# Optimization experiments

Hardware: AMD Instinct MI355X
Metric: run time of the kernel (lower is better)

Reference implementation:

```python
import jax, jax.numpy as jnp
import numpy as np

N_EMBED = 1024
N_HEAD = 16
B, T = 4, 2048
EPS = 1e-5


def setup_inputs() -> dict:
    key = jax.random.key(0)
    ks = jax.random.split(key, 8)
    s = 0.02
    return {
        "x": jax.random.normal(ks[0], (B, T, N_EMBED), dtype=jnp.float32),
        "ln1_w": jnp.ones((N_EMBED,), jnp.float32),
        "ln1_b": jnp.zeros((N_EMBED,), jnp.float32),
        "w_qkv": jax.random.normal(ks[1], (N_EMBED, 3 * N_EMBED), dtype=jnp.float32) * s,
        "b_qkv": jnp.zeros((3 * N_EMBED,), jnp.float32),
        "w_o": jax.random.normal(ks[2], (N_EMBED, N_EMBED), dtype=jnp.float32) * s,
        "b_o": jnp.zeros((N_EMBED,), jnp.float32),
        "ln2_w": jnp.ones((N_EMBED,), jnp.float32),
        "ln2_b": jnp.zeros((N_EMBED,), jnp.float32),
        "w_fc": jax.random.normal(ks[3], (N_EMBED, 4 * N_EMBED), dtype=jnp.float32) * s,
        "b_fc": jnp.zeros((4 * N_EMBED,), jnp.float32),
        "w_proj": jax.random.normal(ks[4], (4 * N_EMBED, N_EMBED), dtype=jnp.float32) * s,
        "b_proj": jnp.zeros((N_EMBED,), jnp.float32),
    }


def _layernorm(x, w, b):
    mu = jnp.mean(x, axis=-1, keepdims=True)
    var = jnp.mean(jnp.square(x - mu), axis=-1, keepdims=True)
    return (x - mu) * jax.lax.rsqrt(var + EPS) * w + b


def _attention(x, w_qkv, b_qkv, w_o, b_o):
    b, t, c = x.shape
    hd = c // N_HEAD
    qkv = x @ w_qkv + b_qkv                      # [B,T,3C]
    q, k, v = jnp.split(qkv, 3, axis=-1)
    # [B,H,T,hd]
    q = q.reshape(b, t, N_HEAD, hd).transpose(0, 2, 1, 3)
    k = k.reshape(b, t, N_HEAD, hd).transpose(0, 2, 1, 3)
    v = v.reshape(b, t, N_HEAD, hd).transpose(0, 2, 1, 3)
    scale = 1.0 / np.sqrt(hd).astype(np.float32)
    scores = jnp.einsum('bhqd,bhkd->bhqk', q, k) * scale  # [B,H,T,T]
    mask = jnp.tril(jnp.ones((t, t), dtype=bool))
    scores = jnp.where(mask, scores, -jnp.inf)
    attn = jax.nn.softmax(scores, axis=-1)
    ctx = jnp.einsum('bhqk,bhkd->bhqd', attn, v)  # [B,H,T,hd]
    ctx = ctx.transpose(0, 2, 1, 3).reshape(b, t, c)
    return ctx @ w_o + b_o


def reference(x, ln1_w, ln1_b, w_qkv, b_qkv, w_o, b_o,
              ln2_w, ln2_b, w_fc, b_fc, w_proj, b_proj):
    # x = x + attn(ln1(x))
    x = x + _attention(_layernorm(x, ln1_w, ln1_b), w_qkv, b_qkv, w_o, b_o)
    # x = x + mlp(ln2(x))
    h = _layernorm(x, ln2_w, ln2_b)
    h = jax.nn.gelu(h @ w_fc + b_fc, approximate=False)
    x = x + (h @ w_proj + b_proj)
    return x
```

## Files before the change

### kernel.cpp

```cpp
#include <hip/hip_runtime.h>
#include <hip/hip_bf16.h>
#include <math.h>

#define N_EMBED 1024
#define N_HEAD 16
#define HD 64
#define BB 4
#define TT 2048
#define NTOK (BB * TT)
#define QKV_LD (3 * N_EMBED)

typedef __bf16 bf16x8 __attribute__((ext_vector_type(8)));
typedef float f32x4 __attribute__((ext_vector_type(4)));

__device__ __forceinline__ unsigned short f2bf(float f) {
    __hip_bfloat16 h = __float2bfloat16(f);
    return __builtin_bit_cast(unsigned short, h);
}

__device__ __forceinline__ void gll16(const unsigned short* g, unsigned short* l) {
    __builtin_amdgcn_global_load_lds(
        (const __attribute__((address_space(1))) void*)g,
        (__attribute__((address_space(3))) void*)l,
        16, 0, 0);
}

__global__ __launch_bounds__(256) void transpose_bf16_kernel(
    const float* __restrict__ in, unsigned short* __restrict__ out, int K, int N) {
    __shared__ float tile[32][33];
    int bx = blockIdx.x * 32;
    int by = blockIdx.y * 32;
    int tx = threadIdx.x, ty = threadIdx.y;
#pragma unroll
    for (int i = ty; i < 32; i += 8)
        tile[i][tx] = in[(size_t)(by + i) * N + bx + tx];
    __syncthreads();
#pragma unroll
    for (int i = ty; i < 32; i += 8)
        out[(size_t)(bx + i) * K + by + tx] = f2bf(tile[tx][i]);
}

__global__ __launch_bounds__(256) void transpose_v_kernel(
    const unsigned short* __restrict__ qkv, unsigned short* __restrict__ vt) {
    __shared__ unsigned short tile[32][33];
    int z = blockIdx.z;
    int b = z >> 4, h = z & 15;
    int t0 = blockIdx.x * 32, d0 = blockIdx.y * 32;
    int tx = threadIdx.x, ty = threadIdx.y;
    const unsigned short* src = qkv + (size_t)(b * TT) * QKV_LD + 2 * N_EMBED + h * HD;
#pragma unroll
    for (int i = ty; i < 32; i += 8)
        tile[i][tx] = src[(size_t)(t0 + i) * QKV_LD + d0 + tx];
    __syncthreads();
    unsigned short* dst = vt + (size_t)z * HD * TT;
#pragma unroll
    for (int i = ty; i < 32; i += 8)
        dst[(size_t)(d0 + i) * TT + t0 + tx] = tile[tx][i];
}

__global__ __launch_bounds__(256) void ln_kernel(
    const float* __restrict__ x, const float* __restrict__ w,
    const float* __restrict__ b, unsigned short* __restrict__ out) {
    int row = blockIdx.x;
    int t = threadIdx.x;
    const float* xr = x + (size_t)row * N_EMBED;
    float4 v = reinterpret_cast<const float4*>(xr)[t];
    float s = v.x + v.y + v.z + v.w;
    float s2 = v.x * v.x + v.y * v.y + v.z * v.z + v.w * v.w;
#pragma unroll
    for (int m = 1; m < 64; m <<= 1) {
        s += __shfl_xor(s, m);
        s2 += __shfl_xor(s2, m);
    }
    __shared__ float red[8];
    int wv = t >> 6, ln = t & 63;
    if (ln == 0) { red[wv] = s; red[wv + 4] = s2; }
    __syncthreads();
    s = red[0] + red[1] + red[2] + red[3];
    s2 = red[4] + red[5] + red[6] + red[7];
    float mu = s * (1.0f / N_EMBED);
    float var = s2 * (1.0f / N_EMBED) - mu * mu;
    float r = rsqrtf(var + 1e-5f);
    float4 wv4 = reinterpret_cast<const float4*>(w)[t];
    float4 bv4 = reinterpret_cast<const float4*>(b)[t];
    ushort4 o;
    o.x = f2bf((v.x - mu) * r * wv4.x + bv4.x);
    o.y = f2bf((v.y - mu) * r * wv4.y + bv4.y);
    o.z = f2bf((v.z - mu) * r * wv4.z + bv4.z);
    o.w = f2bf((v.w - mu) * r * wv4.w + bv4.w);
    *reinterpret_cast<ushort4*>(out + (size_t)row * N_EMBED + t * 4) = o;
}

template <int EPI>
__global__ __launch_bounds__(256) void gemm_kernel(
    const unsigned short* __restrict__ A,
    const unsigned short* __restrict__ BT,
    const float* __restrict__ bias,
    const float* __restrict__ resid,
    float* __restrict__ outf,
    unsigned short* __restrict__ outb,
    int M, int N, int K) {
    __shared__ __align__(16) unsigned short As[3][128 * 32];
    __shared__ __align__(16) unsigned short Bs[3][128 * 32];
    int nbn = N >> 7;
    int nwg = gridDim.x;
    int orig = blockIdx.x;
    int swz = (orig & 7) * (nwg >> 3) + (orig >> 3);
    int bm = swz / nbn, bn = swz % nbn;
    int t = threadIdx.x;
    int lane = t & 63, wv = t >> 6;
    int wm = wv >> 1, wn = wv & 1;
    int mr = lane & 15, kg = lane >> 4;

    f32x4 acc[4][4];
#pragma unroll
    for (int i = 0; i < 4; i++)
#pragma unroll
        for (int j = 0; j < 4; j++) acc[i][j] = (f32x4){0.f, 0.f, 0.f, 0.f};

    int srow = t >> 2, sq = t & 3;
    int sqs = sq ^ ((srow >> 1) & 3);
    const unsigned short* gA1 = A + (size_t)(bm * 128 + srow) * K + sqs * 8;
    const unsigned short* gA2 = gA1 + (size_t)64 * K;
    const unsigned short* gB1 = BT + (size_t)(bn * 128 + srow) * K + sqs * 8;
    const unsigned short* gB2 = gB1 + (size_t)64 * K;
    int w512 = wv * 512;

    auto stageg = [&](int ki, int bi) {
        int k0 = ki << 5;
        gll16(gA1 + k0, As[bi] + w512);
        gll16(gA2 + k0, As[bi] + 2048 + w512);
        gll16(gB1 + k0, Bs[bi] + w512);
        gll16(gB2 + k0, Bs[bi] + 2048 + w512);
    };

    int nk = K >> 5;
    stageg(0, 0);
    stageg(1, 1);

    const int csw = (mr >> 1) & 3;
    for (int ki = 0; ki < nk; ki++) {
        if (ki + 1 < nk) {
            asm volatile("s_waitcnt vmcnt(4)" ::: "memory");
        } else {
            asm volatile("s_waitcnt vmcnt(0)" ::: "memory");
        }
        __builtin_amdgcn_s_barrier();
        if (ki + 2 < nk) stageg(ki + 2, (ki + 2) % 3);

        int cur = ki % 3;
        bf16x8 af[4], bfr[4];
#pragma unroll
        for (int i = 0; i < 4; i++)
            af[i] = *reinterpret_cast<const bf16x8*>(
                &As[cur][(wm * 64 + i * 16 + mr) * 32 + ((kg ^ csw) * 8)]);
#pragma unroll
        for (int j = 0; j < 4; j++)
            bfr[j] = *reinterpret_cast<const bf16x8*>(
                &Bs[cur][(wn * 64 + j * 16 + mr) * 32 + ((kg ^ csw) * 8)]);
#pragma unroll
        for (int i = 0; i < 4; i++)
#pragma unroll
            for (int j = 0; j < 4; j++)
                acc[i][j] = __builtin_amdgcn_mfma_f32_16x16x32_bf16(af[i], bfr[j], acc[i][j], 0, 0, 0);
    }

#pragma unroll
    for (int i = 0; i < 4; i++)
#pragma unroll
        for (int j = 0; j < 4; j++) {
            int n = bn * 128 + wn * 64 + j * 16 + mr;
            float bs = bias[n];
#pragma unroll
            for (int r = 0; r < 4; r++) {
                int m = bm * 128 + wm * 64 + i * 16 + kg * 4 + r;
                size_t idx = (size_t)m * N + n;
                float v = acc[i][j][r] + bs;
                if (EPI == 0) {
                    outb[idx] = f2bf(v);
                } else if (EPI == 1) {
                    outf[idx] = v + resid[idx];
                } else {
                    float g = 0.5f * v * (1.0f + erff(v * 0.70710678118f));
                    outb[idx] = f2bf(g);
                }
            }
        }
}

__global__ __launch_bounds__(256) void attn_kernel(
    const unsigned short* __restrict__ qkv,
    const unsigned short* __restrict__ vt,
    unsigned short* __restrict__ ctx) {
    __shared__ __align__(16) unsigned short Kb[3][4096];
    __shared__ __align__(16) unsigned short Vb[3][4096];
    __shared__ __align__(16) unsigned short PT[8192];
    const float SCL = 0.18033688011112042f;
    int t = threadIdx.x, lane = t & 63, wv = t >> 6;
    int mr = lane & 15, kg = lane >> 4;

    int wid = blockIdx.x;
    int bh = wid & 63, qp2 = wid >> 6;
    int h = bh & 15, b = bh >> 4;

    const unsigned short* qptr = qkv + (size_t)(b * TT) * QKV_LD + h * HD;
    const unsigned short* kp = qptr + N_EMBED;
    const unsigned short* vtp = vt + (size_t)bh * HD * TT;

    int srow[2], scol[2], sbase[2];
#pragma unroll
    for (int i = 0; i < 2; i++) {
        int L = i * 256 + wv * 64 + lane;
        int row = L >> 3, slot = L & 7;
        srow[i] = row;
        scol[i] = (slot ^ (row & 7)) * 8;
        sbase[i] = (i * 256 + wv * 64) * 8;
    }
    const int csw = mr & 7;

    auto stage = [&](int tile, int bi) {
        int kv0 = tile * 64;
#pragma unroll
        for (int i = 0; i < 2; i++) {
            gll16(kp + (size_t)(kv0 + srow[i]) * QKV_LD + scol[i], &Kb[bi][sbase[i]]);
            gll16(vtp + (size_t)srow[i] * TT + kv0 + scol[i], &Vb[bi][sbase[i]]);
        }
    };

    for (int item = 0; item < 2; ++item) {
        int qt = (item == 0) ? qp2 : 15 - qp2;
        int ntiles = 2 * qt + 2;
        int qbase = qt * 128 + wv * 32;

        bf16x8 aq[2][2];
#pragma unroll
        for (int f = 0; f < 2; f++)
#pragma unroll
            for (int c = 0; c < 2; c++)
                aq[f][c] = *reinterpret_cast<const bf16x8*>(
                    qptr + (size_t)(qbase + f * 16 + mr) * QKV_LD + c * 32 + kg * 8);

        f32x4 Oa[2][4];
#pragma unroll
        for (int f = 0; f < 2; f++)
#pragma unroll
            for (int jd = 0; jd < 4; jd++) Oa[f][jd] = (f32x4){0.f, 0.f, 0.f, 0.f};
        float mrow[2] = {-3.0e38f, -3.0e38f};
        float lrow[2] = {0.f, 0.f};

        stage(0, 0);
        stage(1, 1);

        for (int tl = 0; tl < ntiles; ++tl) {
            if (tl + 1 < ntiles) {
                asm volatile("s_waitcnt vmcnt(4)" ::: "memory");
            } else {
                asm volatile("s_waitcnt vmcnt(0)" ::: "memory");
            }
            __builtin_amdgcn_s_barrier();
            int t2 = tl + 2;
            if (t2 < ntiles) stage(t2, t2 % 3);

            int bi = tl % 3;
            int kv0 = tl * 64;
            const unsigned short* Kt = Kb[bi];
            const unsigned short* Vt = Vb[bi];

            f32x4 sf[2][4];
#pragma unroll
            for (int j = 0; j < 4; j++) {
                int rl = j * 16 + mr;
                bf16x8 bk0 = *reinterpret_cast<const bf16x8*>(&Kt[rl * 64 + (kg ^ csw) * 8]);
                bf16x8 bk1 = *reinterpret_cast<const bf16x8*>(&Kt[rl * 64 + ((4 + kg) ^ csw) * 8]);
#pragma unroll
                for (int f = 0; f < 2; f++) {
                    f32x4 s = (f32x4){0.f, 0.f, 0.f, 0.f};
                    s = __builtin_amdgcn_mfma_f32_16x16x32_bf16(bk0, aq[f][0], s, 0, 0, 0);
                    s = __builtin_amdgcn_mfma_f32_16x16x32_bf16(bk1, aq[f][1], s, 0, 0, 0);
                    sf[f][j] = s;
                }
            }

            bool dmask = (tl >= 2 * qt);
#pragma unroll
            for (int f = 0; f < 2; f++) {
                int qrow = qbase + f * 16 + mr;
                int R = wv * 32 + f * 16 + mr;
                float mx = -3.0e38f;
#pragma unroll
                for (int j = 0; j < 4; j++)
#pragma unroll
                    for (int r = 0; r < 4; r++) {
                        float sv = sf[f][j][r] * SCL;
                        if (dmask && (kv0 + j * 16 + kg * 4 + r > qrow)) sv = -3.0e38f;
                        sf[f][j][r] = sv;
                        mx = fmaxf(mx, sv);
                    }
                mx = fmaxf(mx, __shfl_xor(mx, 16));
                mx = fmaxf(mx, __shfl_xor(mx, 32));
                float mn = fmaxf(mrow[f], mx);
                float al = __builtin_amdgcn_exp2f(mrow[f] - mn);
                mrow[f] = mn;
#pragma unroll
                for (int jd = 0; jd < 4; jd++) Oa[f][jd] *= al;
                float ps = 0.f;
#pragma unroll
                for (int j = 0; j < 4; j++)
#pragma unroll
                    for (int r = 0; r < 4; r++) {
                        float p = __builtin_amdgcn_exp2f(sf[f][j][r] - mn);
                        sf[f][j][r] = p;
                        ps += p;
                    }
                ps += __shfl_xor(ps, 16);
                ps += __shfl_xor(ps, 32);
                lrow[f] = lrow[f] * al + ps;
                int rsw = R & 7;
#pragma unroll
                for (int j = 0; j < 4; j++) {
                    unsigned lo = (unsigned)f2bf(sf[f][j][0]) | ((unsigned)f2bf(sf[f][j][1]) << 16);
                    unsigned hi = (unsigned)f2bf(sf[f][j][2]) | ((unsigned)f2bf(sf[f][j][3]) << 16);
                    int cw = 2 * j + (kg >> 1);
                    int addr = R * 64 + ((cw ^ rsw) << 3) + (kg & 1) * 4;
                    uint2 pk; pk.x = lo; pk.y = hi;
                    *reinterpret_cast<uint2*>(&PT[addr]) = pk;
                }
            }

#pragma unroll
            for (int c = 0; c < 2; c++) {
                int R0 = wv * 32 + mr, R1 = R0 + 16;
                bf16x8 pb0 = *reinterpret_cast<const bf16x8*>(
                    &PT[R0 * 64 + (((c * 4 + kg) ^ (R0 & 7)) << 3)]);
                bf16x8 pb1 = *reinterpret_cast<const bf16x8*>(
                    &PT[R1 * 64 + (((c * 4 + kg) ^ (R1 & 7)) << 3)]);
#pragma unroll
                for (int jd = 0; jd < 4; jd++) {
                    int rv = jd * 16 + mr;
                    bf16x8 vf = *reinterpret_cast<const bf16x8*>(
                        &Vt[rv * 64 + (((c * 4 + kg) ^ (rv & 7)) << 3)]);
                    Oa[0][jd] = __builtin_amdgcn_mfma_f32_16x16x32_bf16(vf, pb0, Oa[0][jd], 0, 0, 0);
                    Oa[1][jd] = __builtin_amdgcn_mfma_f32_16x16x32_bf16(vf, pb1, Oa[1][jd], 0, 0, 0);
                }
            }
        }

#pragma unroll
        for (int f = 0; f < 2; f++) {
            float iv = 1.0f / lrow[f];
            int q = qbase + f * 16 + mr;
#pragma unroll
            for (int jd = 0; jd < 4; jd++) {
                ushort4 o;
                o.x = f2bf(Oa[f][jd][0] * iv);
                o.y = f2bf(Oa[f][jd][1] * iv);
                o.z = f2bf(Oa[f][jd][2] * iv);
                o.w = f2bf(Oa[f][jd][3] * iv);
                *reinterpret_cast<ushort4*>(
                    ctx + (size_t)(b * TT + q) * N_EMBED + h * HD + jd * 16 + kg * 4) = o;
            }
        }
        __syncthreads();
    }
}

extern "C" void kernel_launch(void* const* d_in, const int* in_sizes, int n_in,
                              void* d_out, int out_size, void* d_ws, size_t ws_size,
                              hipStream_t stream) {
    const float* x      = (const float*)d_in[0];
    const float* ln1_w  = (const float*)d_in[1];
    const float* ln1_b  = (const float*)d_in[2];
    const float* w_qkv  = (const float*)d_in[3];
    const float* b_qkv  = (const float*)d_in[4];
    const float* w_o    = (const float*)d_in[5];
    const float* b_o    = (const float*)d_in[6];
    const float* ln2_w  = (const float*)d_in[7];
    const float* ln2_b  = (const float*)d_in[8];
    const float* w_fc   = (const float*)d_in[9];
    const float* b_fc   = (const float*)d_in[10];
    const float* w_proj = (const float*)d_in[11];
    const float* b_proj = (const float*)d_in[12];
    float* out = (float*)d_out;

    char* ws = (char*)d_ws;
    size_t off = 0;
    auto alloc = [&](size_t bytes) -> void* {
        void* p = ws + off;
        off += (bytes + 255) & ~(size_t)255;
        return p;
    };
    unsigned short* wqkv_t  = (unsigned short*)alloc((size_t)3072 * 1024 * 2);
    unsigned short* wo_t    = (unsigned short*)alloc((size_t)1024 * 1024 * 2);
    unsigned short* wfc_t   = (unsigned short*)alloc((size_t)4096 * 1024 * 2);
    unsigned short* wproj_t = (unsigned short*)alloc((size_t)1024 * 4096 * 2);
    unsigned short* lnb     = (unsigned short*)alloc((size_t)NTOK * 1024 * 2);
    float*          x1      = (float*)alloc((size_t)NTOK * 1024 * 4);
    unsigned short* qkv     = (unsigned short*)alloc((size_t)NTOK * 3072 * 2);
    unsigned short* ctxb    = (unsigned short*)alloc((size_t)NTOK * 1024 * 2);
    unsigned short* hbuf    = qkv;
    unsigned short* vt      = (unsigned short*)x1;

    dim3 tb32(32, 8);
    transpose_bf16_kernel<<<dim3(3072 / 32, 1024 / 32), tb32, 0, stream>>>(w_qkv, wqkv_t, 1024, 3072);
    transpose_bf16_kernel<<<dim3(1024 / 32, 1024 / 32), tb32, 0, stream>>>(w_o, wo_t, 1024, 1024);
    transpose_bf16_kernel<<<dim3(4096 / 32, 1024 / 32), tb32, 0, stream>>>(w_fc, wfc_t, 1024, 4096);
    transpose_bf16_kernel<<<dim3(1024 / 32, 4096 / 32), tb32, 0, stream>>>(w_proj, wproj_t, 4096, 1024);

    ln_kernel<<<NTOK, 256, 0, stream>>>(x, ln1_w, ln1_b, lnb);
    gemm_kernel<0><<<(NTOK / 128) * (3072 / 128), 256, 0, stream>>>(
        lnb, wqkv_t, b_qkv, nullptr, nullptr, qkv, NTOK, 3072, 1024);
    transpose_v_kernel<<<dim3(TT / 32, HD / 32, BB * N_HEAD), tb32, 0, stream>>>(qkv, vt);
    attn_kernel<<<512, 256, 0, stream>>>(qkv, vt, ctxb);
    gemm_kernel<1><<<(NTOK / 128) * (1024 / 128), 256, 0, stream>>>(
        ctxb, wo_t, b_o, x, x1, nullptr, NTOK, 1024, 1024);
    ln_kernel<<<NTOK, 256, 0, stream>>>(x1, ln2_w, ln2_b, lnb);
    gemm_kernel<2><<<(NTOK / 128) * (4096 / 128), 256, 0, stream>>>(
        lnb, wfc_t, b_fc, nullptr, nullptr, hbuf, NTOK, 4096, 1024);
    gemm_kernel<1><<<(NTOK / 128) * (1024 / 128), 256, 0, stream>>>(
        hbuf, wproj_t, b_proj, x1, out, nullptr, NTOK, 1024, 4096);
}
```

Measured before the change: 425.1 us.

## Enlarge GEMM tiles to 256x256/256x128 with templated warp layout and MFMA priority

Replaces the fixed 128x128 GEMM with a templated kernel where each wave computes a 128x64 output tile (8x4 MFMA accumulators). The QKV and FC GEMMs use 256x256 tiles with 512 threads, and the O and proj GEMMs use 256x128 tiles. The aim is more operand reuse per LDS load and less global traffic per FLOP. It also raises wave priority around the MFMA block with s_setprio. The cost is higher register pressure, since accumulators double, plus more LDS per block and fewer blocks for the N=1024 GEMMs, which may hurt occupancy and tail balance.

```diff
diff --git a/kernel.cpp b/kernel.cpp
--- a/kernel.cpp
+++ b/kernel.cpp
@@ -91,8 +91,8 @@
     *reinterpret_cast<ushort4*>(out + (size_t)row * N_EMBED + t * 4) = o;
 }
 
-template <int EPI>
-__global__ __launch_bounds__(256) void gemm_kernel(
+template <int EPI, int WM, int WN>
+__global__ __launch_bounds__(WM * WN * 64, 2) void gemm256_kernel(
     const unsigned short* __restrict__ A,
     const unsigned short* __restrict__ BT,
     const float* __restrict__ bias,
@@ -100,80 +100,103 @@
     float* __restrict__ outf,
     unsigned short* __restrict__ outb,
     int M, int N, int K) {
-    __shared__ __align__(16) unsigned short As[3][128 * 32];
-    __shared__ __align__(16) unsigned short Bs[3][128 * 32];
-    int nbn = N >> 7;
+    constexpr int BM = WM * 128;
+    constexpr int BN = WN * 64;
+    constexpr int T = WM * WN * 64;
+    constexpr int CA = BM * 4 / T;
+    constexpr int CB = BN * 4 / T;
+    constexpr int CALLS = CA + CB;
+    __shared__ __align__(16) unsigned short As[3][BM * 32];
+    __shared__ __align__(16) unsigned short Bs[3][BN * 32];
+
+    int nbn = N / BN;
     int nwg = gridDim.x;
     int orig = blockIdx.x;
     int swz = (orig & 7) * (nwg >> 3) + (orig >> 3);
     int bm = swz / nbn, bn = swz % nbn;
     int t = threadIdx.x;
     int lane = t & 63, wv = t >> 6;
-    int wm = wv >> 1, wn = wv & 1;
+    int wm = wv / WN, wn = wv % WN;
     int mr = lane & 15, kg = lane >> 4;
 
-    f32x4 acc[4][4];
-#pragma unroll
-    for (int i = 0; i < 4; i++)
+    f32x4 acc[8][4];
+#pragma unroll
+    for (int i = 0; i < 8; i++)
 #pragma unroll
         for (int j = 0; j < 4; j++) acc[i][j] = (f32x4){0.f, 0.f, 0.f, 0.f};
 
-    int srow = t >> 2, sq = t & 3;
-    int sqs = sq ^ ((srow >> 1) & 3);
-    const unsigned short* gA1 = A + (size_t)(bm * 128 + srow) * K + sqs * 8;
-    const unsigned short* gA2 = gA1 + (size_t)64 * K;
-    const unsigned short* gB1 = BT + (size_t)(bn * 128 + srow) * K + sqs * 8;
-    const unsigned short* gB2 = gB1 + (size_t)64 * K;
-    int w512 = wv * 512;
-
-    auto stageg = [&](int ki, int bi) {
+    const unsigned short* srcA[CA];
+    int dstA[CA];
+#pragma unroll
+    for (int c = 0; c < CA; c++) {
+        int L = c * T + wv * 64 + lane;
+        int row = L >> 2, slot = L & 3;
+        srcA[c] = A + (size_t)(bm * BM + row) * K + (slot ^ ((row >> 1) & 3)) * 8;
+        dstA[c] = (c * T + wv * 64) * 8;
+    }
+    const unsigned short* srcB[CB];
+    int dstB[CB];
+#pragma unroll
+    for (int c = 0; c < CB; c++) {
+        int L = c * T + wv * 64 + lane;
+        int row = L >> 2, slot = L & 3;
+        srcB[c] = BT + (size_t)(bn * BN + row) * K + (slot ^ ((row >> 1) & 3)) * 8;
+        dstB[c] = (c * T + wv * 64) * 8;
+    }
+
+    auto stage = [&](int ki, int bi) {
         int k0 = ki << 5;
-        gll16(gA1 + k0, As[bi] + w512);
-        gll16(gA2 + k0, As[bi] + 2048 + w512);
-        gll16(gB1 + k0, Bs[bi] + w512);
-        gll16(gB2 + k0, Bs[bi] + 2048 + w512);
+#pragma unroll
+        for (int c = 0; c < CA; c++) gll16(srcA[c] + k0, As[bi] + dstA[c]);
+#pragma unroll
+        for (int c = 0; c < CB; c++) gll16(srcB[c] + k0, Bs[bi] + dstB[c]);
     };
 
     int nk = K >> 5;
-    stageg(0, 0);
-    stageg(1, 1);
-
-    const int csw = (mr >> 1) & 3;
+    stage(0, 0);
+    stage(1, 1);
+
     for (int ki = 0; ki < nk; ki++) {
         if (ki + 1 < nk) {
-            asm volatile("s_waitcnt vmcnt(4)" ::: "memory");
+            asm volatile("s_waitcnt vmcnt(%0)" ::"n"(CALLS) : "memory");
         } else {
             asm volatile("s_waitcnt vmcnt(0)" ::: "memory");
         }
         __builtin_amdgcn_s_barrier();
-        if (ki + 2 < nk) stageg(ki + 2, (ki + 2) % 3);
+        if (ki + 2 < nk) stage(ki + 2, (ki + 2) % 3);
 
         int cur = ki % 3;
-        bf16x8 af[4], bfr[4];
-#pragma unroll
-        for (int i = 0; i < 4; i++)
+        bf16x8 af[8], bfr[4];
+#pragma unroll
+        for (int i = 0; i < 8; i++) {
+            int row = wm * 128 + i * 16 + mr;
             af[i] = *reinterpret_cast<const bf16x8*>(
-                &As[cur][(wm * 64 + i * 16 + mr) * 32 + ((kg ^ csw) * 8)]);
-#pragma unroll
-        for (int j = 0; j < 4; j++)
+                &As[cur][row * 32 + ((kg ^ ((row >> 1) & 3)) * 8)]);
+        }
+#pragma unroll
+        for (int j = 0; j < 4; j++) {
+            int row = wn * 64 + j * 16 + mr;
             bfr[j] = *reinterpret_cast<const bf16x8*>(
-                &Bs[cur][(wn * 64 + j * 16 + mr) * 32 + ((kg ^ csw) * 8)]);
-#pragma unroll
-        for (int i = 0; i < 4; i++)
+                &Bs[cur][row * 32 + ((kg ^ ((row >> 1) & 3)) * 8)]);
+        }
+        __builtin_amdgcn_s_setprio(1);
+#pragma unroll
+        for (int i = 0; i < 8; i++)
 #pragma unroll
             for (int j = 0; j < 4; j++)
                 acc[i][j] = __builtin_amdgcn_mfma_f32_16x16x32_bf16(af[i], bfr[j], acc[i][j], 0, 0, 0);
-    }
-
-#pragma unroll
-    for (int i = 0; i < 4; i++)
+        __builtin_amdgcn_s_setprio(0);
+    }
+
+#pragma unroll
+    for (int i = 0; i < 8; i++)
 #pragma unroll
         for (int j = 0; j < 4; j++) {
-            int n = bn * 128 + wn * 64 + j * 16 + mr;
+            int n = bn * BN + wn * 64 + j * 16 + mr;
             float bs = bias[n];
 #pragma unroll
             for (int r = 0; r < 4; r++) {
-                int m = bm * 128 + wm * 64 + i * 16 + kg * 4 + r;
+                int m = bm * BM + wm * 128 + i * 16 + kg * 4 + r;
                 size_t idx = (size_t)m * N + n;
                 float v = acc[i][j][r] + bs;
                 if (EPI == 0) {
@@ -407,15 +430,15 @@
     transpose_bf16_kernel<<<dim3(1024 / 32, 4096 / 32), tb32, 0, stream>>>(w_proj, wproj_t, 4096, 1024);
 
     ln_kernel<<<NTOK, 256, 0, stream>>>(x, ln1_w, ln1_b, lnb);
-    gemm_kernel<0><<<(NTOK / 128) * (3072 / 128), 256, 0, stream>>>(
+    gemm256_kernel<0, 2, 4><<<(NTOK / 256) * (3072 / 256), 512, 0, stream>>>(
         lnb, wqkv_t, b_qkv, nullptr, nullptr, qkv, NTOK, 3072, 1024);
     transpose_v_kernel<<<dim3(TT / 32, HD / 32, BB * N_HEAD), tb32, 0, stream>>>(qkv, vt);
     attn_kernel<<<512, 256, 0, stream>>>(qkv, vt, ctxb);
-    gemm_kernel<1><<<(NTOK / 128) * (1024 / 128), 256, 0, stream>>>(
+    gemm256_kernel<1, 2, 2><<<(NTOK / 256) * (1024 / 128), 256, 0, stream>>>(
         ctxb, wo_t, b_o, x, x1, nullptr, NTOK, 1024, 1024);
     ln_kernel<<<NTOK, 256, 0, stream>>>(x1, ln2_w, ln2_b, lnb);
-    gemm_kernel<2><<<(NTOK / 128) * (4096 / 128), 256, 0, stream>>>(
+    gemm256_kernel<2, 2, 4><<<(NTOK / 256) * (4096 / 256), 512, 0, stream>>>(
         lnb, wfc_t, b_fc, nullptr, nullptr, hbuf, NTOK, 4096, 1024);
-    gemm_kernel<1><<<(NTOK / 128) * (1024 / 128), 256, 0, stream>>>(
+    gemm256_kernel<1, 2, 2><<<(NTOK / 256) * (1024 / 128), 256, 0, stream>>>(
         hbuf, wproj_t, b_proj, x1, out, nullptr, NTOK, 1024, 4096);
 }
```

After: 517.9 us. 1.22x slower.

## Fuse V transpose into QKV GEMM epilogue and double-buffer attention K/V

Applied to the files above, without the earlier changes.

Removes the separate V-transpose kernel by having the QKV GEMM write V blocks directly in transposed [b,h,d,t] layout. The attention kernel switches from triple to double buffering of K/V tiles in LDS, issues the next tile's prefetch before the wait, adds a per-tile barrier and raises wave priority around MFMA sections. The fused epilogue writes V with strided 2-byte stores that may coalesce poorly, and the shallower pipeline may expose more load latency.

```diff
diff --git a/kernel.cpp b/kernel.cpp
--- a/kernel.cpp
+++ b/kernel.cpp
@@ -38,24 +38,6 @@
 #pragma unroll
     for (int i = ty; i < 32; i += 8)
         out[(size_t)(bx + i) * K + by + tx] = f2bf(tile[tx][i]);
-}
-
-__global__ __launch_bounds__(256) void transpose_v_kernel(
-    const unsigned short* __restrict__ qkv, unsigned short* __restrict__ vt) {
-    __shared__ unsigned short tile[32][33];
-    int z = blockIdx.z;
-    int b = z >> 4, h = z & 15;
-    int t0 = blockIdx.x * 32, d0 = blockIdx.y * 32;
-    int tx = threadIdx.x, ty = threadIdx.y;
-    const unsigned short* src = qkv + (size_t)(b * TT) * QKV_LD + 2 * N_EMBED + h * HD;
-#pragma unroll
-    for (int i = ty; i < 32; i += 8)
-        tile[i][tx] = src[(size_t)(t0 + i) * QKV_LD + d0 + tx];
-    __syncthreads();
-    unsigned short* dst = vt + (size_t)z * HD * TT;
-#pragma unroll
-    for (int i = ty; i < 32; i += 8)
-        dst[(size_t)(d0 + i) * TT + t0 + tx] = tile[tx][i];
 }
 
 __global__ __launch_bounds__(256) void ln_kernel(
@@ -99,6 +81,7 @@
     const float* __restrict__ resid,
     float* __restrict__ outf,
     unsigned short* __restrict__ outb,
+    unsigned short* __restrict__ vout,
     int M, int N, int K) {
     __shared__ __align__(16) unsigned short As[3][128 * 32];
     __shared__ __align__(16) unsigned short Bs[3][128 * 32];
@@ -165,6 +148,7 @@
                 acc[i][j] = __builtin_amdgcn_mfma_f32_16x16x32_bf16(af[i], bfr[j], acc[i][j], 0, 0, 0);
     }
 
+    bool vblock = (EPI == 3) && (bn * 128 >= 2 * N_EMBED);
 #pragma unroll
     for (int i = 0; i < 4; i++)
 #pragma unroll
@@ -180,9 +164,17 @@
                     outb[idx] = f2bf(v);
                 } else if (EPI == 1) {
                     outf[idx] = v + resid[idx];
-                } else {
+                } else if (EPI == 2) {
                     float g = 0.5f * v * (1.0f + erff(v * 0.70710678118f));
                     outb[idx] = f2bf(g);
+                } else {
+                    if (!vblock) {
+                        outb[idx] = f2bf(v);
+                    } else {
+                        int bI = m >> 11, tt = m & 2047;
+                        int hh = (n >> 6) & 15, d = n & 63;
+                        vout[(size_t)((bI * 16 + hh) * 64 + d) * TT + tt] = f2bf(v);
+                    }
                 }
             }
         }
@@ -192,8 +184,8 @@
     const unsigned short* __restrict__ qkv,
     const unsigned short* __restrict__ vt,
     unsigned short* __restrict__ ctx) {
-    __shared__ __align__(16) unsigned short Kb[3][4096];
-    __shared__ __align__(16) unsigned short Vb[3][4096];
+    __shared__ __align__(16) unsigned short Kb[2][4096];
+    __shared__ __align__(16) unsigned short Vb[2][4096];
     __shared__ __align__(16) unsigned short PT[8192];
     const float SCL = 0.18033688011112042f;
     int t = threadIdx.x, lane = t & 63, wv = t >> 6;
@@ -249,24 +241,23 @@
         float lrow[2] = {0.f, 0.f};
 
         stage(0, 0);
-        stage(1, 1);
 
         for (int tl = 0; tl < ntiles; ++tl) {
+            int bi = tl & 1;
             if (tl + 1 < ntiles) {
+                stage(tl + 1, bi ^ 1);
                 asm volatile("s_waitcnt vmcnt(4)" ::: "memory");
             } else {
                 asm volatile("s_waitcnt vmcnt(0)" ::: "memory");
             }
             __builtin_amdgcn_s_barrier();
-            int t2 = tl + 2;
-            if (t2 < ntiles) stage(t2, t2 % 3);
-
-            int bi = tl % 3;
+
             int kv0 = tl * 64;
             const unsigned short* Kt = Kb[bi];
             const unsigned short* Vt = Vb[bi];
 
             f32x4 sf[2][4];
+            __builtin_amdgcn_s_setprio(1);
 #pragma unroll
             for (int j = 0; j < 4; j++) {
                 int rl = j * 16 + mr;
@@ -280,6 +271,7 @@
                     sf[f][j] = s;
                 }
             }
+            __builtin_amdgcn_s_setprio(0);
 
             bool dmask = (tl >= 2 * qt);
 #pragma unroll
@@ -327,6 +319,7 @@
                 }
             }
 
+            __builtin_amdgcn_s_setprio(1);
 #pragma unroll
             for (int c = 0; c < 2; c++) {
                 int R0 = wv * 32 + mr, R1 = R0 + 16;
@@ -343,6 +336,8 @@
                     Oa[1][jd] = __builtin_amdgcn_mfma_f32_16x16x32_bf16(vf, pb1, Oa[1][jd], 0, 0, 0);
                 }
             }
+            __builtin_amdgcn_s_setprio(0);
+            __builtin_amdgcn_s_barrier();
         }
 
 #pragma unroll
@@ -360,7 +355,6 @@
                     ctx + (size_t)(b * TT + q) * N_EMBED + h * HD + jd * 16 + kg * 4) = o;
             }
         }
-        __syncthreads();
     }
 }
 
@@ -407,15 +401,14 @@
     transpose_bf16_kernel<<<dim3(1024 / 32, 4096 / 32), tb32, 0, stream>>>(w_proj, wproj_t, 4096, 1024);
 
     ln_kernel<<<NTOK, 256, 0, stream>>>(x, ln1_w, ln1_b, lnb);
-    gemm_kernel<0><<<(NTOK / 128) * (3072 / 128), 256, 0, stream>>>(
-        lnb, wqkv_t, b_qkv, nullptr, nullptr, qkv, NTOK, 3072, 1024);
-    transpose_v_kernel<<<dim3(TT / 32, HD / 32, BB * N_HEAD), tb32, 0, stream>>>(qkv, vt);
+    gemm_kernel<3><<<(NTOK / 128) * (3072 / 128), 256, 0, stream>>>(
+        lnb, wqkv_t, b_qkv, nullptr, nullptr, qkv, vt, NTOK, 3072, 1024);
     attn_kernel<<<512, 256, 0, stream>>>(qkv, vt, ctxb);
     gemm_kernel<1><<<(NTOK / 128) * (1024 / 128), 256, 0, stream>>>(
-        ctxb, wo_t, b_o, x, x1, nullptr, NTOK, 1024, 1024);
+        ctxb, wo_t, b_o, x, x1, nullptr, nullptr, NTOK, 1024, 1024);
     ln_kernel<<<NTOK, 256, 0, stream>>>(x1, ln2_w, ln2_b, lnb);
     gemm_kernel<2><<<(NTOK / 128) * (4096 / 128), 256, 0, stream>>>(
-        lnb, wfc_t, b_fc, nullptr, nullptr, hbuf, NTOK, 4096, 1024);
+        lnb, wfc_t, b_fc, nullptr, nullptr, hbuf, nullptr, NTOK, 4096, 1024);
     gemm_kernel<1><<<(NTOK / 128) * (1024 / 128), 256, 0, stream>>>(
-        hbuf, wproj_t, b_proj, x1, out, nullptr, NTOK, 1024, 4096);
-}
+        hbuf, wproj_t, b_proj, x1, out, nullptr, nullptr, NTOK, 1024, 4096);
+}
```

Result: slower. 436.8 us (+2.8%).

## Add 256x256-tile 8-wave pipelined GEMM for QKV and FC projections

Applied to the files above, without the earlier changes.

Adds a new GEMM kernel with 256x256 output tiles, 512 threads (8 waves) and a 64-wide K step split into halves. Loads go through global_load_lds double buffering and are interleaved with MFMA phases, with barriers, sched_barrier and setprio controlling the schedule. The QKV and FC projections now use it, to raise data reuse per tile and overlap loads with compute. The larger tile means fewer workgroups (384 and 512), which risks lower occupancy or poorer wave balance across CUs. The epilogue writes bf16 with strided per-element stores.

```diff
diff --git a/kernel.cpp b/kernel.cpp
--- a/kernel.cpp
+++ b/kernel.cpp
@@ -92,6 +92,131 @@
 }
 
 template <int EPI>
+__global__ __launch_bounds__(512, 2) void gemm8p_kernel(
+    const unsigned short* __restrict__ A,
+    const unsigned short* __restrict__ BT,
+    const float* __restrict__ bias,
+    unsigned short* __restrict__ outb,
+    int M, int N, int K) {
+    __shared__ __align__(16) unsigned short As[32768];
+    __shared__ __align__(16) unsigned short Bs[32768];
+    int nbn = N >> 8;
+    int nwg = gridDim.x;
+    int orig = blockIdx.x;
+    int swz = (orig & 7) * (nwg >> 3) + (orig >> 3);
+    int bm = swz / nbn, bn = swz % nbn;
+    int t = threadIdx.x;
+    int lane = t & 63, wv = t >> 6;
+    int wm = wv >> 2, wn = wv & 3;
+    int mr = lane & 15, kg = lane >> 4;
+
+    f32x4 acc[8][4];
+#pragma unroll
+    for (int i = 0; i < 8; i++)
+#pragma unroll
+        for (int j = 0; j < 4; j++) acc[i][j] = (f32x4){0.f, 0.f, 0.f, 0.f};
+
+    int srow = t & 255;
+    int sch = t >> 8;
+    const unsigned short* Abase = A + (size_t)(bm * 256 + srow) * K + sch * 8;
+    const unsigned short* Bbase = BT + (size_t)(bn * 256 + srow) * K + sch * 8;
+    unsigned short* Adst = As + wv * 512;
+    unsigned short* Bdst = Bs + wv * 512;
+
+    auto stA = [&](int kt, int kh, int buf) {
+        const unsigned short* s = Abase + kt * 64 + kh * 32;
+        unsigned short* d = Adst + buf * 16384 + kh * 8192;
+        gll16(s, d);
+        gll16(s + 16, d + 4096);
+    };
+    auto stB = [&](int kt, int kh, int buf) {
+        const unsigned short* s = Bbase + kt * 64 + kh * 32;
+        unsigned short* d = Bdst + buf * 16384 + kh * 8192;
+        gll16(s, d);
+        gll16(s + 16, d + 4096);
+    };
+    auto ldA = [&](int buf, int kh, int rb) {
+        return *reinterpret_cast<const bf16x8*>(
+            &As[buf * 16384 + kh * 8192 + kg * 2048 + (wm * 128 + rb + mr) * 8]);
+    };
+    auto ldB = [&](int buf, int kh, int j) {
+        return *reinterpret_cast<const bf16x8*>(
+            &Bs[buf * 16384 + kh * 8192 + kg * 2048 + (wn * 64 + j * 16 + mr) * 8]);
+    };
+
+    bf16x8 bf[4];
+
+#define PHASE8(BUF, KH, IH, READB, ...)                                        \
+    {                                                                          \
+        bf16x8 a0 = ldA(BUF, KH, (IH)*64 + 0);                                 \
+        bf16x8 a1 = ldA(BUF, KH, (IH)*64 + 16);                                \
+        bf16x8 a2 = ldA(BUF, KH, (IH)*64 + 32);                                \
+        bf16x8 a3 = ldA(BUF, KH, (IH)*64 + 48);                                \
+        if (READB) {                                                           \
+            bf[0] = ldB(BUF, KH, 0); bf[1] = ldB(BUF, KH, 1);                  \
+            bf[2] = ldB(BUF, KH, 2); bf[3] = ldB(BUF, KH, 3);                  \
+        }                                                                      \
+        __VA_ARGS__;                                                           \
+        __builtin_amdgcn_s_barrier();                                          \
+        asm volatile("s_waitcnt lgkmcnt(0)" ::: "memory");                     \
+        __builtin_amdgcn_sched_barrier(0);                                     \
+        __builtin_amdgcn_s_setprio(1);                                         \
+        _Pragma("unroll") for (int j = 0; j < 4; j++) {                        \
+            acc[(IH)*4 + 0][j] = __builtin_amdgcn_mfma_f32_16x16x32_bf16(a0, bf[j], acc[(IH)*4 + 0][j], 0, 0, 0); \
+            acc[(IH)*4 + 1][j] = __builtin_amdgcn_mfma_f32_16x16x32_bf16(a1, bf[j], acc[(IH)*4 + 1][j], 0, 0, 0); \
+            acc[(IH)*4 + 2][j] = __builtin_amdgcn_mfma_f32_16x16x32_bf16(a2, bf[j], acc[(IH)*4 + 2][j], 0, 0, 0); \
+            acc[(IH)*4 + 3][j] = __builtin_amdgcn_mfma_f32_16x16x32_bf16(a3, bf[j], acc[(IH)*4 + 3][j], 0, 0, 0); \
+        }                                                                      \
+        __builtin_amdgcn_s_setprio(0);                                         \
+        __builtin_amdgcn_s_barrier();                                          \
+    }
+
+    int nk = K >> 6;
+    int nit = nk >> 1;
+
+    stA(0, 0, 0); stB(0, 0, 0);
+    stA(0, 1, 0); stB(0, 1, 0);
+    stA(1, 0, 1); stB(1, 0, 1);
+
+    for (int it = 0; it < nit; ++it) {
+        int T = 2 * it;
+        bool last = (it == nit - 1);
+        asm volatile("s_waitcnt vmcnt(4)" ::: "memory");
+        __builtin_amdgcn_s_barrier();
+        PHASE8(0, 0, 0, 1, stA(T + 1, 1, 1))
+        PHASE8(0, 0, 1, 0, stB(T + 1, 1, 1))
+        PHASE8(0, 1, 0, 1, if (!last) stA(T + 2, 0, 0))
+        PHASE8(0, 1, 1, 0, if (!last) stB(T + 2, 0, 0))
+        if (last) {
+            asm volatile("s_waitcnt vmcnt(0)" ::: "memory");
+        } else {
+            asm volatile("s_waitcnt vmcnt(4)" ::: "memory");
+        }
+        __builtin_amdgcn_s_barrier();
+        PHASE8(1, 0, 0, 1, if (!last) stA(T + 2, 1, 0))
+        PHASE8(1, 0, 1, 0, if (!last) stB(T + 2, 1, 0))
+        PHASE8(1, 1, 0, 1, if (!last) stA(T + 3, 0, 1))
+        PHASE8(1, 1, 1, 0, if (!last) stB(T + 3, 0, 1))
+    }
+#undef PHASE8
+
+#pragma unroll
+    for (int i = 0; i < 8; i++)
+#pragma unroll
+        for (int j = 0; j < 4; j++) {
+            int n = bn * 256 + wn * 64 + j * 16 + mr;
+            float bs = bias[n];
+#pragma unroll
+            for (int r = 0; r < 4; r++) {
+                int m = bm * 256 + wm * 128 + i * 16 + kg * 4 + r;
+                float v = acc[i][j][r] + bs;
+                if (EPI == 2) v = 0.5f * v * (1.0f + erff(v * 0.70710678118f));
+                outb[(size_t)m * N + n] = f2bf(v);
+            }
+        }
+}
+
+template <int EPI>
 __global__ __launch_bounds__(256) void gemm_kernel(
     const unsigned short* __restrict__ A,
     const unsigned short* __restrict__ BT,
@@ -407,15 +532,15 @@
     transpose_bf16_kernel<<<dim3(1024 / 32, 4096 / 32), tb32, 0, stream>>>(w_proj, wproj_t, 4096, 1024);
 
     ln_kernel<<<NTOK, 256, 0, stream>>>(x, ln1_w, ln1_b, lnb);
-    gemm_kernel<0><<<(NTOK / 128) * (3072 / 128), 256, 0, stream>>>(
-        lnb, wqkv_t, b_qkv, nullptr, nullptr, qkv, NTOK, 3072, 1024);
+    gemm8p_kernel<0><<<(NTOK / 256) * (3072 / 256), 512, 0, stream>>>(
+        lnb, wqkv_t, b_qkv, qkv, NTOK, 3072, 1024);
     transpose_v_kernel<<<dim3(TT / 32, HD / 32, BB * N_HEAD), tb32, 0, stream>>>(qkv, vt);
     attn_kernel<<<512, 256, 0, stream>>>(qkv, vt, ctxb);
     gemm_kernel<1><<<(NTOK / 128) * (1024 / 128), 256, 0, stream>>>(
         ctxb, wo_t, b_o, x, x1, nullptr, NTOK, 1024, 1024);
     ln_kernel<<<NTOK, 256, 0, stream>>>(x1, ln2_w, ln2_b, lnb);
-    gemm_kernel<2><<<(NTOK / 128) * (4096 / 128), 256, 0, stream>>>(
-        lnb, wfc_t, b_fc, nullptr, nullptr, hbuf, NTOK, 4096, 1024);
+    gemm8p_kernel<2><<<(NTOK / 256) * (4096 / 256), 512, 0, stream>>>(
+        lnb, wfc_t, b_fc, hbuf, NTOK, 4096, 1024);
     gemm_kernel<1><<<(NTOK / 128) * (1024 / 128), 256, 0, stream>>>(
         hbuf, wproj_t, b_proj, x1, out, nullptr, NTOK, 1024, 4096);
 }
```

Result: slower. 489.8 us (+15.2%).
